# Kernel optimization log

Measured on AMD Instinct MI355X. Metric: run time of the kernel, lower is better.

The kernel has to match this reference:

```python
import jax, jax.numpy as jnp
import numpy as np

N, INC, INN, OUTC, OUTN, MAXD = 8, 64, 20000, 64, 8000, 32


def setup_inputs() -> dict:
    key = jax.random.key(0)
    k0, k1, k2, k3, k4 = jax.random.split(key, 5)
    # adjacency list: outn nodes, degree in [8, 32], padded to MAXD with index 0
    rng = np.random.default_rng(0)
    deg = rng.integers(8, MAXD + 1, size=OUTN)                      # (outn,)
    A_np = rng.integers(0, INN, size=(OUTN, MAXD))                  # (outn, maxD)
    valid = np.arange(MAXD)[None, :] < deg[:, None]
    A_np = np.where(valid, A_np, 0)
    # '_norm' option: mask entries are 1/degree for valid slots, 0 for pad
    mask_np = valid.astype(np.float32) / deg[:, None].astype(np.float32)

    x = jax.random.normal(k0, (N, INC, INN), dtype=jnp.float32)
    # hadamard weight: sqrt(2/inn) * U(-1, 1)
    weight = np.sqrt(2.0 / INN).astype(np.float32) * (
        2.0 * jax.random.uniform(k1, (INC, INN), dtype=jnp.float32) - 1.0)
    # weight_norm Linear(inc, outc): v (outc, inc) direction, g (outc,) magnitude
    ct_v = jax.random.normal(k2, (OUTC, INC), dtype=jnp.float32) * (1.0 / np.sqrt(INC).astype(np.float32))
    ct_g = 0.5 + jax.random.uniform(k3, (OUTC,), dtype=jnp.float32)
    bias = 0.2 * jax.random.normal(k4, (1, OUTC, OUTN), dtype=jnp.float32)
    return {
        'x': x,
        'weight': weight,
        'ct_v': ct_v,
        'ct_g': ct_g,
        'bias': bias,
        'mask': jnp.asarray(mask_np),
        'A': jnp.asarray(A_np, dtype=jnp.int32),
    }


def reference(x, weight, ct_v, ct_g, bias, mask, A):
    # x: (N, inc, inn); weight: (inc, inn)
    xw = x * weight                                   # hadamard
    gathered = xw[:, :, A]                            # (N, inc, outn, maxD) adjacency gather
    pooled = jnp.einsum('bcod,od->bco', gathered, mask)  # degree-normalized masked sum
    # weight_norm: W = g * v / ||v||_row
    W = ct_g[:, None] * ct_v / jnp.linalg.norm(ct_v, axis=1, keepdims=True)  # (outc, inc)
    y = jnp.einsum('bco,kc->bko', pooled, W)          # (N, outc, outn)
    return y + bias
```

## Files before the change

### kernel.cpp

```cpp
#include <hip/hip_runtime.h>
#include <stdint.h>

#define NB   8
#define INC  64
#define INN  20000
#define OUTC 64
#define OUTN 8000
#define MAXD 32
#define NG   16

__device__ __forceinline__ uint32_t pack_bf16_2(float a, float b) {
    uint32_t ua = __float_as_uint(a);
    uint32_t ub = __float_as_uint(b);
    uint32_t ra = (ua + 0x7FFFu + ((ua >> 16) & 1u)) >> 16;
    uint32_t rb = (ub + 0x7FFFu + ((ub >> 16) & 1u)) >> 16;
    return (ra & 0xFFFFu) | (rb << 16);
}

__global__ void prep_kernel(const int* __restrict__ A, const float* __restrict__ mask,
                            const float* __restrict__ ct_v, const float* __restrict__ ct_g,
                            int4* __restrict__ A4, float2* __restrict__ scale2,
                            float* __restrict__ W_T) {
    if (blockIdx.x == 64) {
        int k = threadIdx.x;
        if (k < OUTC) {
            float s = 0.f;
            for (int c = 0; c < INC; ++c) { float v = ct_v[k * INC + c]; s += v * v; }
            float inv = ct_g[k] / sqrtf(s);
            for (int c = 0; c < INC; ++c) W_T[c * OUTC + k] = ct_v[k * INC + c] * inv;
        }
        return;
    }
    int o = blockIdx.x * 128 + threadIdx.x;
    if (o >= OUTN) return;
    const int4* arow = (const int4*)(A + (size_t)o * MAXD);
#pragma unroll
    for (int q = 0; q < 8; ++q) {
        int4 v = arow[q];
        v.x <<= 3; v.y <<= 3; v.z <<= 3; v.w <<= 3;
        A4[(size_t)q * OUTN + o] = v;
    }
    float invdeg = mask[(size_t)o * MAXD];
    float deg    = rintf(1.0f / invdeg);
    scale2[o] = make_float2(invdeg, 32.0f - deg);
}

__global__ __launch_bounds__(1024, 1)
void gather_kernel(const float* __restrict__ x, const float* __restrict__ w,
                   const int4* __restrict__ A4, const float2* __restrict__ scale2,
                   float* __restrict__ pooled) {
    __shared__ __align__(16) uint2 smem[INN];
    int h = blockIdx.x;
    int g = blockIdx.y;
    int b = blockIdx.z;
    int tid = threadIdx.x;
    int c0 = g * 4;

    const float* xb = x + ((size_t)b * INC + c0) * INN;
    const float* wb = w + (size_t)c0 * INN;
    for (int p = tid; p < INN / 4; p += 1024) {
        int i = p * 4;
        float4 xc[4], wc[4];
#pragma unroll
        for (int cl = 0; cl < 4; ++cl) {
            xc[cl] = *(const float4*)(xb + (size_t)cl * INN + i);
            wc[cl] = *(const float4*)(wb + (size_t)cl * INN + i);
        }
        float p0[4] = {xc[0].x * wc[0].x, xc[0].y * wc[0].y, xc[0].z * wc[0].z, xc[0].w * wc[0].w};
        float p1[4] = {xc[1].x * wc[1].x, xc[1].y * wc[1].y, xc[1].z * wc[1].z, xc[1].w * wc[1].w};
        float p2[4] = {xc[2].x * wc[2].x, xc[2].y * wc[2].y, xc[2].z * wc[2].z, xc[2].w * wc[2].w};
        float p3[4] = {xc[3].x * wc[3].x, xc[3].y * wc[3].y, xc[3].z * wc[3].z, xc[3].w * wc[3].w};
        uint4 lo, hi;
        lo.x = pack_bf16_2(p0[0], p1[0]);  lo.y = pack_bf16_2(p2[0], p3[0]);
        lo.z = pack_bf16_2(p0[1], p1[1]);  lo.w = pack_bf16_2(p2[1], p3[1]);
        hi.x = pack_bf16_2(p0[2], p1[2]);  hi.y = pack_bf16_2(p2[2], p3[2]);
        hi.z = pack_bf16_2(p0[3], p1[3]);  hi.w = pack_bf16_2(p2[3], p3[3]);
        uint4* dst = (uint4*)&smem[i];
        dst[0] = lo;
        dst[1] = hi;
    }
    __syncthreads();

    uint2 z0 = smem[0];
    float z00 = __uint_as_float(z0.x << 16);
    float z01 = __uint_as_float(z0.x & 0xFFFF0000u);
    float z02 = __uint_as_float(z0.y << 16);
    float z03 = __uint_as_float(z0.y & 0xFFFF0000u);

    const char* sbase = (const char*)smem;
    int obase = h * (OUTN / 2);
    int oend  = obase + (OUTN / 2);
#pragma unroll
    for (int it = 0; it < 4; ++it) {
        int o = obase + tid + it * 1024;
        if (o < oend) {
            int4 q[8];
#pragma unroll
            for (int dg = 0; dg < 8; ++dg) q[dg] = A4[(size_t)dg * OUTN + o];

            float a0 = 0.f, a1 = 0.f, a2 = 0.f, a3 = 0.f;
#pragma unroll
            for (int dg = 0; dg < 8; ++dg) {
                uint2 v0 = *(const uint2*)(sbase + q[dg].x);
                uint2 v1 = *(const uint2*)(sbase + q[dg].y);
                uint2 v2 = *(const uint2*)(sbase + q[dg].z);
                uint2 v3 = *(const uint2*)(sbase + q[dg].w);
                a0 += __uint_as_float(v0.x << 16);
                a1 += __uint_as_float(v0.x & 0xFFFF0000u);
                a2 += __uint_as_float(v0.y << 16);
                a3 += __uint_as_float(v0.y & 0xFFFF0000u);
                a0 += __uint_as_float(v1.x << 16);
                a1 += __uint_as_float(v1.x & 0xFFFF0000u);
                a2 += __uint_as_float(v1.y << 16);
                a3 += __uint_as_float(v1.y & 0xFFFF0000u);
                a0 += __uint_as_float(v2.x << 16);
                a1 += __uint_as_float(v2.x & 0xFFFF0000u);
                a2 += __uint_as_float(v2.y << 16);
                a3 += __uint_as_float(v2.y & 0xFFFF0000u);
                a0 += __uint_as_float(v3.x << 16);
                a1 += __uint_as_float(v3.x & 0xFFFF0000u);
                a2 += __uint_as_float(v3.y << 16);
                a3 += __uint_as_float(v3.y & 0xFFFF0000u);
            }
            float2 sc = scale2[o];
            a0 = (a0 - sc.y * z00) * sc.x;
            a1 = (a1 - sc.y * z01) * sc.x;
            a2 = (a2 - sc.y * z02) * sc.x;
            a3 = (a3 - sc.y * z03) * sc.x;
            pooled[((size_t)(b * OUTC + c0 + 0)) * OUTN + o] = a0;
            pooled[((size_t)(b * OUTC + c0 + 1)) * OUTN + o] = a1;
            pooled[((size_t)(b * OUTC + c0 + 2)) * OUTN + o] = a2;
            pooled[((size_t)(b * OUTC + c0 + 3)) * OUTN + o] = a3;
        }
    }
}

__global__ __launch_bounds__(256)
void out_kernel(float* io, const float* __restrict__ W_T,
                const float* __restrict__ bias) {
    __shared__ __align__(16) float sp[INC][128];
    __shared__ __align__(16) float sw[INC][OUTC];
    int obase = blockIdx.x * 128;
    int b     = blockIdx.y;

    const float* pb = io + (size_t)b * INC * OUTN;
    for (int idx = threadIdx.x; idx < INC * 32; idx += 256) {
        int c  = idx >> 5;
        int q  = idx & 31;
        int o4 = obase + q * 4;
        float4 v = (o4 < OUTN) ? *(const float4*)(pb + (size_t)c * OUTN + o4)
                               : make_float4(0.f, 0.f, 0.f, 0.f);
        *(float4*)(&sp[c][q * 4]) = v;
    }
    for (int idx = threadIdx.x; idx < (INC * OUTC) / 4; idx += 256) {
        ((float4*)sw)[idx] = ((const float4*)W_T)[idx];
    }
    __syncthreads();

    int t   = threadIdx.x;
    int kt  = t >> 4;
    int ot0 = (t & 15) * 8;
    int k0  = kt * 4;

    float acc[4][8];
#pragma unroll
    for (int kk = 0; kk < 4; ++kk) {
#pragma unroll
        for (int jh = 0; jh < 2; ++jh) {
            int o4 = obase + ot0 + jh * 4;
            float4 bv = (o4 < OUTN)
                ? *(const float4*)(bias + (size_t)(k0 + kk) * OUTN + o4)
                : make_float4(0.f, 0.f, 0.f, 0.f);
            acc[kk][jh * 4 + 0] = bv.x;
            acc[kk][jh * 4 + 1] = bv.y;
            acc[kk][jh * 4 + 2] = bv.z;
            acc[kk][jh * 4 + 3] = bv.w;
        }
    }

#pragma unroll 4
    for (int c = 0; c < INC; ++c) {
        float4 w4  = *(const float4*)(&sw[c][k0]);
        float4 pa  = *(const float4*)(&sp[c][ot0]);
        float4 pb4 = *(const float4*)(&sp[c][ot0 + 4]);
        float p[8] = {pa.x, pa.y, pa.z, pa.w, pb4.x, pb4.y, pb4.z, pb4.w};
        float wv[4] = {w4.x, w4.y, w4.z, w4.w};
#pragma unroll
        for (int kk = 0; kk < 4; ++kk)
#pragma unroll
            for (int j = 0; j < 8; ++j)
                acc[kk][j] += wv[kk] * p[j];
    }

    int o0 = obase + ot0;
    if (o0 < OUTN) {
#pragma unroll
        for (int kk = 0; kk < 4; ++kk) {
            float4 s0 = make_float4(acc[kk][0], acc[kk][1], acc[kk][2], acc[kk][3]);
            float4 s1 = make_float4(acc[kk][4], acc[kk][5], acc[kk][6], acc[kk][7]);
            float* dst = io + ((size_t)(b * OUTC + k0 + kk)) * OUTN + o0;
            *(float4*)(dst)     = s0;
            *(float4*)(dst + 4) = s1;
        }
    }
}

extern "C" void kernel_launch(void* const* d_in, const int* in_sizes, int n_in,
                              void* d_out, int out_size, void* d_ws, size_t ws_size,
                              hipStream_t stream) {
    const float* x    = (const float*)d_in[0];
    const float* w    = (const float*)d_in[1];
    const float* ct_v = (const float*)d_in[2];
    const float* ct_g = (const float*)d_in[3];
    const float* bias = (const float*)d_in[4];
    const float* mask = (const float*)d_in[5];
    const int*   A    = (const int*)d_in[6];
    float* y = (float*)d_out;

    char* ws = (char*)d_ws;
    int4*   A4     = (int4*)(ws);
    float2* scale2 = (float2*)(ws + 1024000);
    float*  W_T    = (float*)(ws + 1088000);

    prep_kernel<<<65, 128, 0, stream>>>(A, mask, ct_v, ct_g, A4, scale2, W_T);
    gather_kernel<<<dim3(2, NG, NB), 1024, 0, stream>>>(x, w, A4, scale2, y);
    out_kernel<<<dim3(63, NB), 256, 0, stream>>>(y, W_T, bias);
}
```

Before: 47.74 us.

## Halve channels per gather block and pack adjacency indices into 16-bit pairs

Each gather block now stages two bf16 channels per node (4 bytes) instead of four (8 bytes), halving LDS use to about 80KB so more blocks can be resident per CU, and the grid doubles to 32 channel groups. The adjacency list is packed as two 16-bit indices per word, halving index traffic and registers. In exchange, x*w products are staged per pair of channels, so each index is loaded and each LDS gather is issued twice as often across the grid.

After: 52.38 us. 9.7% more time.

```diff
diff --git a/kernel.cpp b/kernel.cpp
--- a/kernel.cpp
+++ b/kernel.cpp
@@ -7,7 +7,6 @@
 #define OUTC 64
 #define OUTN 8000
 #define MAXD 32
-#define NG   16
 
 __device__ __forceinline__ uint32_t pack_bf16_2(float a, float b) {
     uint32_t ua = __float_as_uint(a);
@@ -19,7 +18,7 @@
 
 __global__ void prep_kernel(const int* __restrict__ A, const float* __restrict__ mask,
                             const float* __restrict__ ct_v, const float* __restrict__ ct_g,
-                            int4* __restrict__ A4, float2* __restrict__ scale2,
+                            uint4* __restrict__ AQ, float2* __restrict__ scale2,
                             float* __restrict__ W_T) {
     if (blockIdx.x == 64) {
         int k = threadIdx.x;
@@ -35,57 +34,52 @@
     if (o >= OUTN) return;
     const int4* arow = (const int4*)(A + (size_t)o * MAXD);
 #pragma unroll
-    for (int q = 0; q < 8; ++q) {
-        int4 v = arow[q];
-        v.x <<= 3; v.y <<= 3; v.z <<= 3; v.w <<= 3;
-        A4[(size_t)q * OUTN + o] = v;
+    for (int j = 0; j < 4; ++j) {
+        int4 v0 = arow[2 * j];
+        int4 v1 = arow[2 * j + 1];
+        uint4 pk;
+        pk.x = (uint32_t)v0.x | ((uint32_t)v0.y << 16);
+        pk.y = (uint32_t)v0.z | ((uint32_t)v0.w << 16);
+        pk.z = (uint32_t)v1.x | ((uint32_t)v1.y << 16);
+        pk.w = (uint32_t)v1.z | ((uint32_t)v1.w << 16);
+        AQ[(size_t)j * OUTN + o] = pk;
     }
     float invdeg = mask[(size_t)o * MAXD];
     float deg    = rintf(1.0f / invdeg);
     scale2[o] = make_float2(invdeg, 32.0f - deg);
 }
 
-__global__ __launch_bounds__(1024, 1)
+__global__ __launch_bounds__(1024, 8)
 void gather_kernel(const float* __restrict__ x, const float* __restrict__ w,
-                   const int4* __restrict__ A4, const float2* __restrict__ scale2,
+                   const uint4* __restrict__ AQ, const float2* __restrict__ scale2,
                    float* __restrict__ pooled) {
-    __shared__ __align__(16) uint2 smem[INN];
+    __shared__ __align__(16) uint32_t smem[INN];
     int h = blockIdx.x;
     int g = blockIdx.y;
     int b = blockIdx.z;
     int tid = threadIdx.x;
-    int c0 = g * 4;
+    int c0 = g * 2;
 
     const float* xb = x + ((size_t)b * INC + c0) * INN;
     const float* wb = w + (size_t)c0 * INN;
     for (int p = tid; p < INN / 4; p += 1024) {
         int i = p * 4;
-        float4 xc[4], wc[4];
-#pragma unroll
-        for (int cl = 0; cl < 4; ++cl) {
-            xc[cl] = *(const float4*)(xb + (size_t)cl * INN + i);
-            wc[cl] = *(const float4*)(wb + (size_t)cl * INN + i);
-        }
-        float p0[4] = {xc[0].x * wc[0].x, xc[0].y * wc[0].y, xc[0].z * wc[0].z, xc[0].w * wc[0].w};
-        float p1[4] = {xc[1].x * wc[1].x, xc[1].y * wc[1].y, xc[1].z * wc[1].z, xc[1].w * wc[1].w};
-        float p2[4] = {xc[2].x * wc[2].x, xc[2].y * wc[2].y, xc[2].z * wc[2].z, xc[2].w * wc[2].w};
-        float p3[4] = {xc[3].x * wc[3].x, xc[3].y * wc[3].y, xc[3].z * wc[3].z, xc[3].w * wc[3].w};
-        uint4 lo, hi;
-        lo.x = pack_bf16_2(p0[0], p1[0]);  lo.y = pack_bf16_2(p2[0], p3[0]);
-        lo.z = pack_bf16_2(p0[1], p1[1]);  lo.w = pack_bf16_2(p2[1], p3[1]);
-        hi.x = pack_bf16_2(p0[2], p1[2]);  hi.y = pack_bf16_2(p2[2], p3[2]);
-        hi.z = pack_bf16_2(p0[3], p1[3]);  hi.w = pack_bf16_2(p2[3], p3[3]);
-        uint4* dst = (uint4*)&smem[i];
-        dst[0] = lo;
-        dst[1] = hi;
+        float4 x0 = *(const float4*)(xb + i);
+        float4 x1 = *(const float4*)(xb + INN + i);
+        float4 w0 = *(const float4*)(wb + i);
+        float4 w1 = *(const float4*)(wb + INN + i);
+        uint4 pk;
+        pk.x = pack_bf16_2(x0.x * w0.x, x1.x * w1.x);
+        pk.y = pack_bf16_2(x0.y * w0.y, x1.y * w1.y);
+        pk.z = pack_bf16_2(x0.z * w0.z, x1.z * w1.z);
+        pk.w = pack_bf16_2(x0.w * w0.w, x1.w * w1.w);
+        *(uint4*)&smem[i] = pk;
     }
     __syncthreads();
 
-    uint2 z0 = smem[0];
-    float z00 = __uint_as_float(z0.x << 16);
-    float z01 = __uint_as_float(z0.x & 0xFFFF0000u);
-    float z02 = __uint_as_float(z0.y << 16);
-    float z03 = __uint_as_float(z0.y & 0xFFFF0000u);
+    uint32_t z = smem[0];
+    float z0 = __uint_as_float(z << 16);
+    float z1 = __uint_as_float(z & 0xFFFF0000u);
 
     const char* sbase = (const char*)smem;
     int obase = h * (OUTN / 2);
@@ -94,43 +88,31 @@
     for (int it = 0; it < 4; ++it) {
         int o = obase + tid + it * 1024;
         if (o < oend) {
-            int4 q[8];
-#pragma unroll
-            for (int dg = 0; dg < 8; ++dg) q[dg] = A4[(size_t)dg * OUTN + o];
-
-            float a0 = 0.f, a1 = 0.f, a2 = 0.f, a3 = 0.f;
-#pragma unroll
-            for (int dg = 0; dg < 8; ++dg) {
-                uint2 v0 = *(const uint2*)(sbase + q[dg].x);
-                uint2 v1 = *(const uint2*)(sbase + q[dg].y);
-                uint2 v2 = *(const uint2*)(sbase + q[dg].z);
-                uint2 v3 = *(const uint2*)(sbase + q[dg].w);
-                a0 += __uint_as_float(v0.x << 16);
-                a1 += __uint_as_float(v0.x & 0xFFFF0000u);
-                a2 += __uint_as_float(v0.y << 16);
-                a3 += __uint_as_float(v0.y & 0xFFFF0000u);
-                a0 += __uint_as_float(v1.x << 16);
-                a1 += __uint_as_float(v1.x & 0xFFFF0000u);
-                a2 += __uint_as_float(v1.y << 16);
-                a3 += __uint_as_float(v1.y & 0xFFFF0000u);
-                a0 += __uint_as_float(v2.x << 16);
-                a1 += __uint_as_float(v2.x & 0xFFFF0000u);
-                a2 += __uint_as_float(v2.y << 16);
-                a3 += __uint_as_float(v2.y & 0xFFFF0000u);
-                a0 += __uint_as_float(v3.x << 16);
-                a1 += __uint_as_float(v3.x & 0xFFFF0000u);
-                a2 += __uint_as_float(v3.y << 16);
-                a3 += __uint_as_float(v3.y & 0xFFFF0000u);
+            uint32_t q[16];
+#pragma unroll
+            for (int j = 0; j < 4; ++j) {
+                uint4 v = AQ[(size_t)j * OUTN + o];
+                q[j * 4 + 0] = v.x; q[j * 4 + 1] = v.y;
+                q[j * 4 + 2] = v.z; q[j * 4 + 3] = v.w;
+            }
+            float a0 = 0.f, a1 = 0.f;
+#pragma unroll
+            for (int p = 0; p < 16; ++p) {
+                uint32_t u   = q[p];
+                int off0 = (int)(u & 0xFFFFu) << 2;
+                int off1 = (int)(u >> 16) << 2;
+                uint32_t v0 = *(const uint32_t*)(sbase + off0);
+                uint32_t v1 = *(const uint32_t*)(sbase + off1);
+                a0 += __uint_as_float(v0 << 16);
+                a1 += __uint_as_float(v0 & 0xFFFF0000u);
+                a0 += __uint_as_float(v1 << 16);
+                a1 += __uint_as_float(v1 & 0xFFFF0000u);
             }
             float2 sc = scale2[o];
-            a0 = (a0 - sc.y * z00) * sc.x;
-            a1 = (a1 - sc.y * z01) * sc.x;
-            a2 = (a2 - sc.y * z02) * sc.x;
-            a3 = (a3 - sc.y * z03) * sc.x;
+            a0 = (a0 - sc.y * z0) * sc.x;
+            a1 = (a1 - sc.y * z1) * sc.x;
             pooled[((size_t)(b * OUTC + c0 + 0)) * OUTN + o] = a0;
             pooled[((size_t)(b * OUTC + c0 + 1)) * OUTN + o] = a1;
-            pooled[((size_t)(b * OUTC + c0 + 2)) * OUTN + o] = a2;
-            pooled[((size_t)(b * OUTC + c0 + 3)) * OUTN + o] = a3;
         }
     }
 }
@@ -218,11 +200,11 @@
     float* y = (float*)d_out;
 
     char* ws = (char*)d_ws;
-    int4*   A4     = (int4*)(ws);
-    float2* scale2 = (float2*)(ws + 1024000);
-    float*  W_T    = (float*)(ws + 1088000);
-
-    prep_kernel<<<65, 128, 0, stream>>>(A, mask, ct_v, ct_g, A4, scale2, W_T);
-    gather_kernel<<<dim3(2, NG, NB), 1024, 0, stream>>>(x, w, A4, scale2, y);
+    uint4*  AQ     = (uint4*)(ws);
+    float2* scale2 = (float2*)(ws + 512000);
+    float*  W_T    = (float*)(ws + 576000);
+
+    prep_kernel<<<65, 128, 0, stream>>>(A, mask, ct_v, ct_g, AQ, scale2, W_T);
+    gather_kernel<<<dim3(2, 32, NB), 1024, 0, stream>>>(x, w, AQ, scale2, y);
     out_kernel<<<dim3(63, NB), 256, 0, stream>>>(y, W_T, bias);
 }
```
